# Kernel tuning notes

Measured on AMD Instinct MI355X. Metric: run time of the kernel, lower is better.

The kernel has to match this reference:

```python
import jax, jax.numpy as jnp
import numpy as np


def setup_inputs() -> dict:
    key = jax.random.key(0)
    k1, k2, k3 = jax.random.split(key, 3)
    x = jax.random.normal(k1, (16, 224, 224, 96), dtype=jnp.float32)
    # Single shared single-channel kernel [kh, kw, 1, mult] applied to every channel
    kernel = jax.random.normal(k2, (3, 3, 1, 2), dtype=jnp.float32) * 0.1
    bias = jax.random.normal(k3, (192,), dtype=jnp.float32) * 0.1
    return {"x": x, "kernel": kernel, "bias": bias}


def reference(x, kernel, bias):
    # x: [B, H, W, C] channels_last; kernel: [kh, kw, 1, mult]; bias: [C*mult]
    B, H, W, C = x.shape
    mult = kernel.shape[-1]
    # The original folds channels into batch and applies the SAME single-channel
    # conv to every channel; equivalent fused form: grouped conv with the kernel
    # tiled across groups. Output channel ordering is c*mult + m, matching the
    # original reshape [B, C, H', W', mult] -> transpose -> [B, H', W', C*mult].
    k_full = jnp.tile(kernel, (1, 1, 1, C))  # [kh, kw, 1, C*mult]
    out = jax.lax.conv_general_dilated(
        x, k_full,
        window_strides=(1, 1),
        padding="SAME",
        rhs_dilation=(1, 1),
        dimension_numbers=("NHWC", "HWIO", "NHWC"),
        feature_group_count=C,
    )
    return out + bias  # bias broadcast over [1,1,1,C*mult]
```

## Files before the change

### kernel.cpp

```cpp
#include <hip/hip_runtime.h>


#define BATCH 16
#define H 224
#define W 224
#define C 96
#define CG (C / 4)
#define CO (C * 2)
#define XT 8

__global__ __launch_bounds__(CG * XT) void dwconv_kernel(
    const float* __restrict__ x,
    const float* __restrict__ k,
    const float* __restrict__ bias,
    float* __restrict__ out)
{
    const int cg = threadIdx.x;
    const int xo = blockIdx.x * XT + threadIdx.y;
    const int y  = blockIdx.y;
    const int b  = blockIdx.z;

    float w[3][3][2];
#pragma unroll
    for (int dy = 0; dy < 3; ++dy)
#pragma unroll
        for (int dx = 0; dx < 3; ++dx)
#pragma unroll
            for (int m = 0; m < 2; ++m)
                w[dy][dx][m] = k[(dy * 3 + dx) * 2 + m];

    float4 accA = make_float4(0.f, 0.f, 0.f, 0.f);
    float4 accB = make_float4(0.f, 0.f, 0.f, 0.f);

    const float* xb = x + ((size_t)b * H * W) * C + (size_t)cg * 4;

    const bool interior = (y >= 1) & (y <= H - 2) & (xo >= 1) & (xo <= W - 2);

    if (interior) {
#pragma unroll
        for (int dy = 0; dy < 3; ++dy) {
            const float* row = xb + ((size_t)(y + dy - 1) * W + (xo - 1)) * C;
#pragma unroll
            for (int dx = 0; dx < 3; ++dx) {
                const float4 v = *(const float4*)(row + (size_t)dx * C);
                const float w0 = w[dy][dx][0], w1 = w[dy][dx][1];
                accA.x += v.x * w0;  accA.y += v.x * w1;
                accA.z += v.y * w0;  accA.w += v.y * w1;
                accB.x += v.z * w0;  accB.y += v.z * w1;
                accB.z += v.w * w0;  accB.w += v.w * w1;
            }
        }
    } else {
#pragma unroll
        for (int dy = 0; dy < 3; ++dy) {
            const int yy = y + dy - 1;
            if (yy < 0 || yy >= H) continue;
#pragma unroll
            for (int dx = 0; dx < 3; ++dx) {
                const int xx = xo + dx - 1;
                if (xx < 0 || xx >= W) continue;
                const float4 v = *(const float4*)(xb + ((size_t)yy * W + xx) * C);
                const float w0 = w[dy][dx][0], w1 = w[dy][dx][1];
                accA.x += v.x * w0;  accA.y += v.x * w1;
                accA.z += v.y * w0;  accA.w += v.y * w1;
                accB.x += v.z * w0;  accB.y += v.z * w1;
                accB.z += v.w * w0;  accB.w += v.w * w1;
            }
        }
    }

    const float4 bA = ((const float4*)bias)[2 * cg + 0];
    const float4 bB = ((const float4*)bias)[2 * cg + 1];
    accA.x += bA.x; accA.y += bA.y; accA.z += bA.z; accA.w += bA.w;
    accB.x += bB.x; accB.y += bB.y; accB.z += bB.z; accB.w += bB.w;

    float4* o = (float4*)(out + (((size_t)b * H + y) * W + xo) * CO + (size_t)cg * 8);
    o[0] = accA;
    o[1] = accB;
}

extern "C" void kernel_launch(void* const* d_in, const int* in_sizes, int n_in,
                              void* d_out, int out_size, void* d_ws, size_t ws_size,
                              hipStream_t stream) {
    const float* x    = (const float*)d_in[0];
    const float* k    = (const float*)d_in[1];
    const float* bias = (const float*)d_in[2];
    float* out = (float*)d_out;

    dim3 block(CG, XT, 1);
    dim3 grid(W / XT, H, BATCH);
    hipLaunchKernelGGL(dwconv_kernel, grid, block, 0, stream, x, k, bias, out);
}
```

Before: 898.0 us.

## Tile 8 output rows per thread with register row reuse and nontemporal stores

Each thread now computes 8 consecutive output rows, loading each input row once and applying it to up to three accumulators, so global reads drop from 9 to about 3.75 float4 loads per output. Edge handling is split into a templated x-edge path for the first and last block columns. Outputs are written with nontemporal stores to avoid polluting cache. In exchange, register use grows (16 float4 accumulators) and the grid shrinks eightfold in y, which may reduce occupancy and parallelism.

```diff
diff --git a/kernel.cpp b/kernel.cpp
--- a/kernel.cpp
+++ b/kernel.cpp
@@ -8,6 +8,90 @@
 #define CG (C / 4)
 #define CO (C * 2)
 #define XT 8
+#define YT 8
+
+typedef float fvec4 __attribute__((ext_vector_type(4)));
+
+__device__ __forceinline__ float4 ld4(const float* p) { return *(const float4*)p; }
+
+__device__ __forceinline__ void st4_nt(float* p, float4 v) {
+    fvec4 t; t.x = v.x; t.y = v.y; t.z = v.z; t.w = v.w;
+    __builtin_nontemporal_store(t, (fvec4*)p);
+}
+
+template <bool XEDGE>
+__device__ __forceinline__ void conv_tile(
+    const float* __restrict__ xb,
+    const float* __restrict__ k,
+    const float* __restrict__ bias,
+    float* __restrict__ out,
+    int b, int y0, int xo, int cg)
+{
+    float w[3][3][2];
+#pragma unroll
+    for (int dy = 0; dy < 3; ++dy)
+#pragma unroll
+        for (int dx = 0; dx < 3; ++dx)
+#pragma unroll
+            for (int m = 0; m < 2; ++m)
+                w[dy][dx][m] = k[(dy * 3 + dx) * 2 + m];
+
+    float4 accA[YT], accB[YT];
+#pragma unroll
+    for (int r = 0; r < YT; ++r) {
+        accA[r] = make_float4(0.f, 0.f, 0.f, 0.f);
+        accB[r] = make_float4(0.f, 0.f, 0.f, 0.f);
+    }
+
+#pragma unroll
+    for (int iy = 0; iy < YT + 2; ++iy) {
+        const int yy = y0 + iy - 1;
+        if ((unsigned)yy >= (unsigned)H) continue;
+        const float* row = xb + ((size_t)yy * W + (xo - 1)) * C;
+        float4 va, vb, vc;
+        if (XEDGE) {
+            va = (xo >= 1)     ? ld4(row)         : make_float4(0.f, 0.f, 0.f, 0.f);
+            vb =                 ld4(row + C);
+            vc = (xo <= W - 2) ? ld4(row + 2 * C) : make_float4(0.f, 0.f, 0.f, 0.f);
+        } else {
+            va = ld4(row);
+            vb = ld4(row + C);
+            vc = ld4(row + 2 * C);
+        }
+#pragma unroll
+        for (int dy = 0; dy < 3; ++dy) {
+            const int r = iy - dy;
+            if (r < 0 || r >= YT) continue;
+            const float q00 = w[dy][0][0], q01 = w[dy][0][1];
+            const float q10 = w[dy][1][0], q11 = w[dy][1][1];
+            const float q20 = w[dy][2][0], q21 = w[dy][2][1];
+            accA[r].x += va.x * q00; accA[r].y += va.x * q01;
+            accA[r].z += va.y * q00; accA[r].w += va.y * q01;
+            accB[r].x += va.z * q00; accB[r].y += va.z * q01;
+            accB[r].z += va.w * q00; accB[r].w += va.w * q01;
+            accA[r].x += vb.x * q10; accA[r].y += vb.x * q11;
+            accA[r].z += vb.y * q10; accA[r].w += vb.y * q11;
+            accB[r].x += vb.z * q10; accB[r].y += vb.z * q11;
+            accB[r].z += vb.w * q10; accB[r].w += vb.w * q11;
+            accA[r].x += vc.x * q20; accA[r].y += vc.x * q21;
+            accA[r].z += vc.y * q20; accA[r].w += vc.y * q21;
+            accB[r].x += vc.z * q20; accB[r].y += vc.z * q21;
+            accB[r].z += vc.w * q20; accB[r].w += vc.w * q21;
+        }
+    }
+
+    const float4 bA = ((const float4*)bias)[2 * cg + 0];
+    const float4 bB = ((const float4*)bias)[2 * cg + 1];
+#pragma unroll
+    for (int r = 0; r < YT; ++r) {
+        float4 oa = accA[r], ob = accB[r];
+        oa.x += bA.x; oa.y += bA.y; oa.z += bA.z; oa.w += bA.w;
+        ob.x += bB.x; ob.y += bB.y; ob.z += bB.z; ob.w += bB.w;
+        float* o = out + (((size_t)b * H + (y0 + r)) * W + xo) * CO + (size_t)cg * 8;
+        st4_nt(o + 0, oa);
+        st4_nt(o + 4, ob);
+    }
+}
 
 __global__ __launch_bounds__(CG * XT) void dwconv_kernel(
     const float* __restrict__ x,
@@ -17,66 +101,15 @@
 {
     const int cg = threadIdx.x;
     const int xo = blockIdx.x * XT + threadIdx.y;
-    const int y  = blockIdx.y;
+    const int y0 = blockIdx.y * YT;
     const int b  = blockIdx.z;
 
-    float w[3][3][2];
-#pragma unroll
-    for (int dy = 0; dy < 3; ++dy)
-#pragma unroll
-        for (int dx = 0; dx < 3; ++dx)
-#pragma unroll
-            for (int m = 0; m < 2; ++m)
-                w[dy][dx][m] = k[(dy * 3 + dx) * 2 + m];
+    const float* xb = x + (size_t)b * H * W * C + (size_t)cg * 4;
 
-    float4 accA = make_float4(0.f, 0.f, 0.f, 0.f);
-    float4 accB = make_float4(0.f, 0.f, 0.f, 0.f);
-
-    const float* xb = x + ((size_t)b * H * W) * C + (size_t)cg * 4;
-
-    const bool interior = (y >= 1) & (y <= H - 2) & (xo >= 1) & (xo <= W - 2);
-
-    if (interior) {
-#pragma unroll
-        for (int dy = 0; dy < 3; ++dy) {
-            const float* row = xb + ((size_t)(y + dy - 1) * W + (xo - 1)) * C;
-#pragma unroll
-            for (int dx = 0; dx < 3; ++dx) {
-                const float4 v = *(const float4*)(row + (size_t)dx * C);
-                const float w0 = w[dy][dx][0], w1 = w[dy][dx][1];
-                accA.x += v.x * w0;  accA.y += v.x * w1;
-                accA.z += v.y * w0;  accA.w += v.y * w1;
-                accB.x += v.z * w0;  accB.y += v.z * w1;
-                accB.z += v.w * w0;  accB.w += v.w * w1;
-            }
-        }
-    } else {
-#pragma unroll
-        for (int dy = 0; dy < 3; ++dy) {
-            const int yy = y + dy - 1;
-            if (yy < 0 || yy >= H) continue;
-#pragma unroll
-            for (int dx = 0; dx < 3; ++dx) {
-                const int xx = xo + dx - 1;
-                if (xx < 0 || xx >= W) continue;
-                const float4 v = *(const float4*)(xb + ((size_t)yy * W + xx) * C);
-                const float w0 = w[dy][dx][0], w1 = w[dy][dx][1];
-                accA.x += v.x * w0;  accA.y += v.x * w1;
-                accA.z += v.y * w0;  accA.w += v.y * w1;
-                accB.x += v.z * w0;  accB.y += v.z * w1;
-                accB.z += v.w * w0;  accB.w += v.w * w1;
-            }
-        }
-    }
-
-    const float4 bA = ((const float4*)bias)[2 * cg + 0];
-    const float4 bB = ((const float4*)bias)[2 * cg + 1];
-    accA.x += bA.x; accA.y += bA.y; accA.z += bA.z; accA.w += bA.w;
-    accB.x += bB.x; accB.y += bB.y; accB.z += bB.z; accB.w += bB.w;
-
-    float4* o = (float4*)(out + (((size_t)b * H + y) * W + xo) * CO + (size_t)cg * 8);
-    o[0] = accA;
-    o[1] = accB;
+    if (blockIdx.x == 0 || blockIdx.x == gridDim.x - 1)
+        conv_tile<true>(xb, k, bias, out, b, y0, xo, cg);
+    else
+        conv_tile<false>(xb, k, bias, out, b, y0, xo, cg);
 }
 
 extern "C" void kernel_launch(void* const* d_in, const int* in_sizes, int n_in,
@@ -88,6 +121,6 @@
     float* out = (float*)d_out;
 
     dim3 block(CG, XT, 1);
-    dim3 grid(W / XT, H, BATCH);
+    dim3 grid(W / XT, H / YT, BATCH);
     hipLaunchKernelGGL(dwconv_kernel, grid, block, 0, stream, x, k, bias, out);
 }
```

After: 873.9 us. 1.03x faster.
